# Optimization experiments

Hardware: AMD Instinct MI355X
Metric: run time of the kernel (lower is better)

Reference implementation:

```python
import jax, jax.numpy as jnp
import numpy as np

DIM = 256
H = 4
HD = DIM // H          # head_dim = 64
B = 4
N = 2048
M = 3                  # number of modalities
TEMP = 0.07
EPS = 1e-5             # torch LayerNorm eps


def _layernorm(x, g, b):
    mu = jnp.mean(x, axis=-1, keepdims=True)
    var = jnp.var(x, axis=-1, keepdims=True)  # biased, matches torch
    return (x - mu) / jnp.sqrt(var + EPS) * g + b


def setup_inputs() -> dict:
    key = jax.random.key(0)
    ks = jax.random.split(key, 8)
    s = 0.02
    return {
        "m0": jax.random.normal(ks[0], (B, N, DIM), jnp.float32),
        "m1": jax.random.normal(ks[1], (B, N, DIM), jnp.float32),
        "m2": jax.random.normal(ks[2], (B, N, DIM), jnp.float32),
        # torch Linear weights are [out, in]; applied as x @ W.T
        "Wq": jax.random.normal(ks[3], (DIM, DIM), jnp.float32) * s,
        "Wk": jax.random.normal(ks[4], (DIM, DIM), jnp.float32) * s,
        "Wv": jax.random.normal(ks[5], (DIM, DIM), jnp.float32) * s,
        "g1": jnp.ones((DIM,), jnp.float32),
        "be1": jnp.zeros((DIM,), jnp.float32),
        "W1": jax.random.normal(ks[6], (4 * DIM, DIM), jnp.float32) * s,
        "bm1": jnp.zeros((4 * DIM,), jnp.float32),
        "W2": jax.random.normal(ks[7], (DIM, 4 * DIM), jnp.float32) * s,
        "bm2": jnp.zeros((DIM,), jnp.float32),
        "g2": jnp.ones((DIM,), jnp.float32),
        "be2": jnp.zeros((DIM,), jnp.float32),
    }


def reference(m0, m1, m2, Wq, Wk, Wv, g1, be1, W1, bm1, W2, bm2, g2, be2):
    mods = jnp.stack([m0, m1, m2])  # [M, B, N, D]

    def proj(W):
        # x @ W.T, split heads -> [M, B, H, N, HD]
        y = jnp.einsum('mbnd,ed->mbne', mods, W)
        return y.reshape(M, B, N, H, HD).transpose(0, 1, 3, 2, 4)

    q, k, v = proj(Wq), proj(Wk), proj(Wv)
    scale = 1.0 / np.sqrt(HD).astype(np.float32)

    pair_loss = jnp.float32(0.0)
    updates = []
    for i in range(M):  # small fixed modality loop
        upd = jnp.zeros((B, N, DIM), mods.dtype)
        for j in range(M):
            # [B, H, N, N] cross-modal scores
            sim = jnp.einsum('bhnd,bhmd->bhnm', q[i], k[j]) * scale
            attn = jax.nn.softmax(sim, axis=-1)
            if i != j:
                diag = jnp.diagonal(sim, axis1=-2, axis2=-1)      # [B, H, N]
                lse = jax.nn.logsumexp(sim / TEMP, axis=-1)       # [B, H, N]
                pair_loss = pair_loss + jnp.mean(-diag + lse)
            au = jnp.einsum('bhnm,bhmd->bhnd', attn, v[j])
            upd = upd + au.transpose(0, 2, 1, 3).reshape(B, N, DIM)
        updates.append(upd)

    # original accumulates the pairwise loss once per outer modality, each
    # time divided by M*(M-1)  ->  total = M * pair_loss / (M*(M-1))
    total_loss = M * pair_loss / (M * (M - 1))

    outs = []
    for m in range(M):
        x = mods[m] + updates[m]
        x = _layernorm(x, g1, be1)
        h = jax.nn.gelu(x @ W1.T + bm1, approximate=False)  # exact GELU like torch
        x = x + (h @ W2.T + bm2)
        x = _layernorm(x, g2, be2)
        outs.append(x)

    return (outs[0], outs[1], outs[2], total_loss)
```

## Files before the change

### kernel.cpp

```cpp
#include <hip/hip_runtime.h>


typedef float f32x2 __attribute__((ext_vector_type(2)));
typedef float f32x4 __attribute__((ext_vector_type(4)));
typedef float f32x16 __attribute__((ext_vector_type(16)));
typedef __bf16 bf16x8 __attribute__((ext_vector_type(8)));
typedef unsigned int u32x2 __attribute__((ext_vector_type(2)));
typedef unsigned int u32x4 __attribute__((ext_vector_type(4)));
typedef unsigned short bfu4 __attribute__((ext_vector_type(4)));
typedef unsigned short bfu;

#define MFMA32(a, b, c) __builtin_amdgcn_mfma_f32_32x32x16_bf16(a, b, c, 0, 0, 0)

#define NTOK 2048
#define DIMM 256
#define HDIM 64
#define DFF 1024
#define OUT_LOSS 6291456
#define INVT 14.285714285714286f
#define LN2F 0.6931471805599453f
#define LOG2EF 1.4426950408889634f

#define EXP2F(x) __builtin_amdgcn_exp2f(x)
#define LOG2F(x) __builtin_amdgcn_logf(x)

__device__ __forceinline__ bfu f2bf(float f) {
  unsigned u = __float_as_uint(f);
  u += 0x7FFFu + ((u >> 16) & 1u);
  return (bfu)(u >> 16);
}
__device__ __forceinline__ float frombf(bfu v) {
  return __uint_as_float(((unsigned)v) << 16);
}

__device__ __forceinline__ bf16x8 ldfrag(const bfu* p) {
  return __builtin_bit_cast(bf16x8, *reinterpret_cast<const u32x4*>(p));
}

__device__ __forceinline__ unsigned pkbf(float lo, float hi) {
  unsigned d;
  asm("v_cvt_pk_bf16_f32 %0, %1, %2" : "=v"(d) : "v"(lo), "v"(hi));
  return d;
}
__device__ __forceinline__ void swap32u(unsigned& a, unsigned& b) {
  asm("v_permlane32_swap_b32 %0, %1" : "+v"(a), "+v"(b));
}
__device__ __forceinline__ float red32_add(float x) {
  float y = x;
  asm("v_permlane32_swap_b32 %0, %1" : "+v"(x), "+v"(y));
  return x + y;
}
__device__ __forceinline__ float red32_max(float x) {
  float y = x;
  asm("v_permlane32_swap_b32 %0, %1" : "+v"(x), "+v"(y));
  return fmaxf(x, y);
}

__global__ __launch_bounds__(256) void k_cvt_all(
    const float* __restrict__ m0, const float* __restrict__ m1,
    const float* __restrict__ m2, const float* __restrict__ Wq,
    const float* __restrict__ Wk, const float* __restrict__ Wv,
    const float* __restrict__ W1, const float* __restrict__ W2,
    bfu* __restrict__ Xb, bfu* __restrict__ Wqkv,
    bfu* __restrict__ W1b, bfu* __restrict__ W2b) {
  const int bid = blockIdx.x, tid = threadIdx.x;
  const float* src;
  bfu* dst;
  int idx;
  if (bid < 6144) {
    const int seg = bid >> 11;
    src = (seg == 0) ? m0 : (seg == 1 ? m1 : m2);
    dst = Xb + (size_t)seg * 2097152;
    idx = (bid & 2047) * 256 + tid;
  } else if (bid < 6336) {
    const int wseg = (bid - 6144) >> 6;
    src = (wseg == 0) ? Wq : (wseg == 1 ? Wk : Wv);
    dst = Wqkv + (size_t)wseg * 65536;
    idx = ((bid - 6144) & 63) * 256 + tid;
  } else if (bid < 6592) {
    src = W1; dst = W1b; idx = (bid - 6336) * 256 + tid;
  } else {
    src = W2; dst = W2b; idx = (bid - 6592) * 256 + tid;
  }
  f32x4 v = reinterpret_cast<const f32x4*>(src)[idx];
  bfu4 o;
  o[0] = f2bf(v[0]); o[1] = f2bf(v[1]); o[2] = f2bf(v[2]); o[3] = f2bf(v[3]);
  reinterpret_cast<bfu4*>(dst)[idx] = o;
}

#define RROW(r) (((r) & 3) + 8 * ((r) >> 2) + 4 * hi)

__global__ __launch_bounds__(256) void k_proj(const bfu* __restrict__ Xb,
                                              const bfu* __restrict__ Wcat,
                                              bfu* __restrict__ Qb,
                                              bfu* __restrict__ Kb,
                                              bfu* __restrict__ VTb) {
  __shared__ __align__(16) bfu sA[128][72];
  __shared__ __align__(16) bfu sB[128][72];
  const int tid = threadIdx.x;
  const int lane = tid & 63, w = tid >> 6;
  const int l31 = lane & 31, hi = lane >> 5, hi8 = hi * 8;
  const int wm = w >> 1, wn = w & 1;
  const int row0 = blockIdx.x * 128;
  const int col0 = blockIdx.y * 128;
  const bfu* Ap = Xb + (size_t)row0 * 256;
  const bfu* Bp = Wcat + (size_t)col0 * 256;
  f32x16 acc00 = {}, acc01 = {}, acc10 = {}, acc11 = {};
  u32x4 rA[4], rB[4];
#pragma unroll
  for (int t = 0; t < 4; ++t) {
    const int c = tid + 256 * t;
    rA[t] = *reinterpret_cast<const u32x4*>(Ap + (size_t)(c >> 3) * 256 + (c & 7) * 8);
    rB[t] = *reinterpret_cast<const u32x4*>(Bp + (size_t)(c >> 3) * 256 + (c & 7) * 8);
  }
#pragma unroll
  for (int ks = 0; ks < 4; ++ks) {
    __syncthreads();
#pragma unroll
    for (int t = 0; t < 4; ++t) {
      const int c = tid + 256 * t;
      *reinterpret_cast<u32x4*>(&sA[c >> 3][(c & 7) * 8]) = rA[t];
      *reinterpret_cast<u32x4*>(&sB[c >> 3][(c & 7) * 8]) = rB[t];
    }
    __syncthreads();
    if (ks < 3) {
      const int k0 = (ks + 1) * 64;
#pragma unroll
      for (int t = 0; t < 4; ++t) {
        const int c = tid + 256 * t;
        rA[t] = *reinterpret_cast<const u32x4*>(Ap + (size_t)(c >> 3) * 256 + k0 + (c & 7) * 8);
        rB[t] = *reinterpret_cast<const u32x4*>(Bp + (size_t)(c >> 3) * 256 + k0 + (c & 7) * 8);
      }
    }
#pragma unroll
    for (int kk = 0; kk < 4; ++kk) {
      bf16x8 a0 = ldfrag(&sA[wm * 64 + l31][kk * 16 + hi8]);
      bf16x8 a1 = ldfrag(&sA[wm * 64 + 32 + l31][kk * 16 + hi8]);
      bf16x8 b0 = ldfrag(&sB[wn * 64 + l31][kk * 16 + hi8]);
      bf16x8 b1 = ldfrag(&sB[wn * 64 + 32 + l31][kk * 16 + hi8]);
      acc00 = MFMA32(a0, b0, acc00);
      acc01 = MFMA32(a0, b1, acc01);
      acc10 = MFMA32(a1, b0, acc10);
      acc11 = MFMA32(a1, b1, acc11);
    }
  }
  const int mb = row0 >> 11;
  const int cb = col0 + wn * 64;
  const int which = cb >> 8;
  const int h = (cb >> 6) & 3;
  const size_t obase = ((size_t)mb * 4 + h) * ((size_t)NTOK * HDIM);
  const int tokb = (row0 & 2047) + wm * 64;
  const float qs = (which == 0) ? 0.125f * LOG2EF : 1.0f;
#define STORE_QK(ACC, MT, NT)                                                 \
  {                                                                           \
    bfu* dst = (which ? Kb : Qb) + obase;                                     \
    _Pragma("unroll") for (int r = 0; r < 16; ++r) {                          \
      const int tok = tokb + (MT) * 32 + RROW(r);                             \
      dst[(size_t)tok * 64 + (NT) * 32 + l31] = f2bf((ACC)[r] * qs);          \
    }                                                                         \
  }
#define STORE_VT(ACC, MT, NT)                                                 \
  {                                                                           \
    _Pragma("unroll") for (int g = 0; g < 4; ++g) {                           \
      bfu4 pk;                                                                \
      _Pragma("unroll") for (int q = 0; q < 4; ++q) pk[q] = f2bf((ACC)[4 * g + q]); \
      const int tok = tokb + (MT) * 32 + 8 * g + 4 * hi;                      \
      *reinterpret_cast<bfu4*>(                                               \
          &VTb[obase + (size_t)((NT) * 32 + l31) * NTOK + tok]) = pk;         \
    }                                                                         \
  }
  if (which < 2) {
    STORE_QK(acc00, 0, 0) STORE_QK(acc01, 0, 1)
    STORE_QK(acc10, 1, 0) STORE_QK(acc11, 1, 1)
  } else {
    STORE_VT(acc00, 0, 0) STORE_VT(acc01, 0, 1)
    STORE_VT(acc10, 1, 0) STORE_VT(acc11, 1, 1)
  }
}

__global__ __launch_bounds__(256) void k_ffn1(const bfu* __restrict__ x1b,
                                              const bfu* __restrict__ W1b,
                                              const float* __restrict__ bm1,
                                              bfu* __restrict__ hb) {
  __shared__ __align__(16) bfu sA[128][72];
  __shared__ __align__(16) bfu sB[128][72];
  const int tid = threadIdx.x;
  const int lane = tid & 63, w = tid >> 6;
  const int l31 = lane & 31, hi = lane >> 5, hi8 = hi * 8;
  const int wm = w >> 1, wn = w & 1;
  const int row0 = blockIdx.x * 128;
  const int col0 = blockIdx.y * 128;
  const bfu* Ap = x1b + (size_t)row0 * 256;
  const bfu* Bp = W1b + (size_t)col0 * 256;
  f32x16 acc00 = {}, acc01 = {}, acc10 = {}, acc11 = {};
  u32x4 rA[4], rB[4];
#pragma unroll
  for (int t = 0; t < 4; ++t) {
    const int c = tid + 256 * t;
    rA[t] = *reinterpret_cast<const u32x4*>(Ap + (size_t)(c >> 3) * 256 + (c & 7) * 8);
    rB[t] = *reinterpret_cast<const u32x4*>(Bp + (size_t)(c >> 3) * 256 + (c & 7) * 8);
  }
#pragma unroll
  for (int ks = 0; ks < 4; ++ks) {
    __syncthreads();
#pragma unroll
    for (int t = 0; t < 4; ++t) {
      const int c = tid + 256 * t;
      *reinterpret_cast<u32x4*>(&sA[c >> 3][(c & 7) * 8]) = rA[t];
      *reinterpret_cast<u32x4*>(&sB[c >> 3][(c & 7) * 8]) = rB[t];
    }
    __syncthreads();
    if (ks < 3) {
      const int k0 = (ks + 1) * 64;
#pragma unroll
      for (int t = 0; t < 4; ++t) {
        const int c = tid + 256 * t;
        rA[t] = *reinterpret_cast<const u32x4*>(Ap + (size_t)(c >> 3) * 256 + k0 + (c & 7) * 8);
        rB[t] = *reinterpret_cast<const u32x4*>(Bp + (size_t)(c >> 3) * 256 + k0 + (c & 7) * 8);
      }
    }
#pragma unroll
    for (int kk = 0; kk < 4; ++kk) {
      bf16x8 a0 = ldfrag(&sA[wm * 64 + l31][kk * 16 + hi8]);
      bf16x8 a1 = ldfrag(&sA[wm * 64 + 32 + l31][kk * 16 + hi8]);
      bf16x8 b0 = ldfrag(&sB[wn * 64 + l31][kk * 16 + hi8]);
      bf16x8 b1 = ldfrag(&sB[wn * 64 + 32 + l31][kk * 16 + hi8]);
      acc00 = MFMA32(a0, b0, acc00);
      acc01 = MFMA32(a0, b1, acc01);
      acc10 = MFMA32(a1, b0, acc10);
      acc11 = MFMA32(a1, b1, acc11);
    }
  }
  const int tokb = row0 + wm * 64;
#define STORE_H(ACC, MT, NT)                                                  \
  {                                                                           \
    const int e = col0 + wn * 64 + (NT) * 32 + l31;                           \
    const float bias = bm1[e];                                                \
    _Pragma("unroll") for (int r = 0; r < 16; ++r) {                          \
      const int tok = tokb + (MT) * 32 + RROW(r);                             \
      float v = (ACC)[r] + bias;                                              \
      v = 0.5f * v * (1.0f + erff(v * 0.70710678118f));                       \
      hb[(size_t)tok * DFF + e] = f2bf(v);                                    \
    }                                                                         \
  }
  STORE_H(acc00, 0, 0) STORE_H(acc01, 0, 1)
  STORE_H(acc10, 1, 0) STORE_H(acc11, 1, 1)
}

__global__ __launch_bounds__(256) void k_ffn2(const bfu* __restrict__ hb,
                                              const bfu* __restrict__ W2b,
                                              const float* __restrict__ bm2,
                                              const bfu* __restrict__ x1b,
                                              float* __restrict__ x2f) {
  __shared__ __align__(16) bfu sA[128][72];
  __shared__ __align__(16) bfu sB[64][72];
  const int tid = threadIdx.x;
  const int lane = tid & 63, w = tid >> 6;
  const int l31 = lane & 31, hi = lane >> 5, hi8 = hi * 8;
  const int row0 = blockIdx.x * 128;
  const int col0 = blockIdx.y * 64;
  const bfu* Ap = hb + (size_t)row0 * DFF;
  const bfu* Bp = W2b + (size_t)col0 * DFF;
  f32x16 acc0 = {}, acc1 = {};
  u32x4 rA[4], rB[2];
#pragma unroll
  for (int t = 0; t < 4; ++t) {
    const int c = tid + 256 * t;
    rA[t] = *reinterpret_cast<const u32x4*>(Ap + (size_t)(c >> 3) * DFF + (c & 7) * 8);
  }
#pragma unroll
  for (int t = 0; t < 2; ++t) {
    const int c = tid + 256 * t;
    rB[t] = *reinterpret_cast<const u32x4*>(Bp + (size_t)(c >> 3) * DFF + (c & 7) * 8);
  }
  for (int ks = 0; ks < 16; ++ks) {
    __syncthreads();
#pragma unroll
    for (int t = 0; t < 4; ++t) {
      const int c = tid + 256 * t;
      *reinterpret_cast<u32x4*>(&sA[c >> 3][(c & 7) * 8]) = rA[t];
    }
#pragma unroll
    for (int t = 0; t < 2; ++t) {
      const int c = tid + 256 * t;
      *reinterpret_cast<u32x4*>(&sB[c >> 3][(c & 7) * 8]) = rB[t];
    }
    __syncthreads();
    if (ks < 15) {
      const int k0 = (ks + 1) * 64;
#pragma unroll
      for (int t = 0; t < 4; ++t) {
        const int c = tid + 256 * t;
        rA[t] = *reinterpret_cast<const u32x4*>(Ap + (size_t)(c >> 3) * DFF + k0 + (c & 7) * 8);
      }
#pragma unroll
      for (int t = 0; t < 2; ++t) {
        const int c = tid + 256 * t;
        rB[t] = *reinterpret_cast<const u32x4*>(Bp + (size_t)(c >> 3) * DFF + k0 + (c & 7) * 8);
      }
    }
#pragma unroll
    for (int kk = 0; kk < 4; ++kk) {
      bf16x8 a = ldfrag(&sA[w * 32 + l31][kk * 16 + hi8]);
      bf16x8 b0 = ldfrag(&sB[l31][kk * 16 + hi8]);
      bf16x8 b1 = ldfrag(&sB[32 + l31][kk * 16 + hi8]);
      acc0 = MFMA32(a, b0, acc0);
      acc1 = MFMA32(a, b1, acc1);
    }
  }
  const int tokb = row0 + w * 32;
#define STORE_Y(ACC, NT)                                                      \
  {                                                                           \
    const int e = col0 + (NT) * 32 + l31;                                     \
    const float bias = bm2[e];                                                \
    _Pragma("unroll") for (int r = 0; r < 16; ++r) {                          \
      const int tok = tokb + RROW(r);                                         \
      x2f[(size_t)tok * DIMM + e] =                                           \
          (ACC)[r] + bias + frombf(x1b[(size_t)tok * DIMM + e]);              \
    }                                                                         \
  }
  STORE_Y(acc0, 0) STORE_Y(acc1, 1)
}

__global__ __launch_bounds__(256, 3) void k_attn(const bfu* __restrict__ Qb,
                                                 const bfu* __restrict__ Kb,
                                                 const bfu* __restrict__ VTb,
                                                 bfu* __restrict__ upd3,
                                                 float* __restrict__ lossbuf) {
  __shared__ __align__(16) bfu sK[2][64][72];
  __shared__ __align__(16) bfu sV[2][64][72];
  __shared__ float sRed[4];
  const int tid = threadIdx.x;
  const int lane = tid & 63, w = tid >> 6;
  const int l31 = lane & 31, hi = lane >> 5;
  const int hi8 = hi * 8;
  const int qt = blockIdx.x, bh = blockIdx.y, ij = blockIdx.z;
  const int i = ij / 3, j = ij % 3;
  const bool wl = (i != j);
  const int b = bh >> 2, h = bh & 3;
  const int q0 = qt * 128 + w * 32;
  const int q = q0 + l31;
  const int ktd = q0 >> 6;
  const size_t plane = (size_t)NTOK * HDIM;
  const size_t qoff = (((size_t)i * 4 + b) * 4 + h) * plane;
  const size_t kvoff = (((size_t)j * 4 + b) * 4 + h) * plane;
  const bfu* Kp = Kb + kvoff;
  const bfu* Vp = VTb + kvoff;
  const int r0 = tid >> 2, c0 = (tid & 3) * 2;

  bf16x8 qf[4];
#pragma unroll
  for (int c = 0; c < 4; ++c)
    qf[c] = ldfrag(Qb + qoff + (size_t)q * HDIM + c * 16 + hi8);

  float lossacc = 0.0f;
  float mrun = -1e30f, lrun = 0.0f, l2run = 0.0f;
  f32x16 O0 = {}, O1 = {};
  u32x4 pk0, pk1, pv0, pv1;

#define ISSUE_TILE(K0)                                                       \
    {                                                                        \
      const bfu* kp_ = Kp + (size_t)((K0) + r0) * HDIM + c0 * 8;             \
      pk0 = *reinterpret_cast<const u32x4*>(kp_);                            \
      pk1 = *reinterpret_cast<const u32x4*>(kp_ + 8);                        \
      const bfu* vp_ = Vp + (size_t)r0 * NTOK + (K0) + c0 * 8;               \
      pv0 = *reinterpret_cast<const u32x4*>(vp_);                            \
      pv1 = *reinterpret_cast<const u32x4*>(vp_ + 8);                        \
    }
#define WRITE_TILE(BUF)                                                      \
    {                                                                        \
      *reinterpret_cast<u32x4*>(&sK[BUF][r0][c0 * 8]) = pk0;                 \
      *reinterpret_cast<u32x4*>(&sK[BUF][r0][c0 * 8 + 8]) = pk1;             \
      *reinterpret_cast<u32x4*>(&sV[BUF][r0][c0 * 8]) = pv0;                 \
      *reinterpret_cast<u32x4*>(&sV[BUF][r0][c0 * 8 + 8]) = pv1;             \
    }

  ISSUE_TILE(0);
  WRITE_TILE(0);
  __syncthreads();
  int cur = 0;

  for (int kt = 0; kt < 32; ++kt) {
    if (kt < 31) ISSUE_TILE((kt + 1) * 64);

    f32x16 S0 = {}, S1 = {};
    __builtin_amdgcn_s_setprio(1);
#pragma unroll
    for (int c = 0; c < 4; ++c) {
      bf16x8 a0 = ldfrag(&sK[cur][l31][c * 16 + hi8]);
      bf16x8 a1 = ldfrag(&sK[cur][32 + l31][c * 16 + hi8]);
      S0 = MFMA32(a0, qf[c], S0);
      S1 = MFMA32(a1, qf[c], S1);
    }
    __builtin_amdgcn_s_setprio(0);

    if (wl) {
      if (kt == ktd) {
#pragma unroll
        for (int r = 0; r < 16; ++r) {
          const int klow = (r & 3) + 8 * (r >> 2) + 4 * hi;
          const float sv = (w & 1) ? S1[r] : S0[r];
          if (klow == l31) lossacc -= sv * LN2F;
        }
      }
      float pmax = -1e30f;
#pragma unroll
      for (int r = 0; r < 16; ++r) pmax = fmaxf(pmax, fmaxf(S0[r], S1[r]));
      pmax = red32_max(pmax);
      if (__any(pmax > mrun + 1.9f)) {
        const float mnew = fmaxf(mrun, pmax);
        l2run *= EXP2F((mrun - mnew) * INVT);
        mrun = mnew;
      }
    }

    const float mI = mrun * INVT;
    f32x2 psv = {};
    f32x2 p2v = {};
#pragma unroll
    for (int r = 0; r < 16; ++r) {
      const float e0 = EXP2F(S0[r]), e1 = EXP2F(S1[r]);
      f32x2 ev; ev[0] = e0; ev[1] = e1;
      psv += ev;
      if (wl) {
        f32x2 pv2;
        pv2[0] = EXP2F(fmaf(S0[r], INVT, -mI));
        pv2[1] = EXP2F(fmaf(S1[r], INVT, -mI));
        p2v += pv2;
      }
      S0[r] = e0; S1[r] = e1;
    }
    lrun += red32_add(psv[0] + psv[1]);
    if (wl) l2run += red32_add(p2v[0] + p2v[1]);

    __builtin_amdgcn_s_setprio(1);
#pragma unroll
    for (int c = 0; c < 4; ++c) {
      const int half = c >> 1, sub = c & 1;
      unsigned q01, q23, q45, q67;
      if (half == 0) {
        q01 = pkbf(S0[sub * 8 + 0], S0[sub * 8 + 1]);
        q23 = pkbf(S0[sub * 8 + 2], S0[sub * 8 + 3]);
        q45 = pkbf(S0[sub * 8 + 4], S0[sub * 8 + 5]);
        q67 = pkbf(S0[sub * 8 + 6], S0[sub * 8 + 7]);
      } else {
        q01 = pkbf(S1[sub * 8 + 0], S1[sub * 8 + 1]);
        q23 = pkbf(S1[sub * 8 + 2], S1[sub * 8 + 3]);
        q45 = pkbf(S1[sub * 8 + 4], S1[sub * 8 + 5]);
        q67 = pkbf(S1[sub * 8 + 6], S1[sub * 8 + 7]);
      }
      swap32u(q01, q45);
      swap32u(q23, q67);
      u32x4 bb; bb[0] = q01; bb[1] = q23; bb[2] = q45; bb[3] = q67;
      const bf16x8 pb = __builtin_bit_cast(bf16x8, bb);
      bf16x8 a0 = ldfrag(&sV[cur][l31][c * 16 + hi8]);
      bf16x8 a1 = ldfrag(&sV[cur][32 + l31][c * 16 + hi8]);
      O0 = MFMA32(a0, pb, O0);
      O1 = MFMA32(a1, pb, O1);
    }
    __builtin_amdgcn_s_setprio(0);

    if (kt < 31) WRITE_TILE(cur ^ 1);
    __syncthreads();
    cur ^= 1;
  }

  const float inv = 1.0f / lrun;
  bfu* up = upd3 + ((size_t)((j * 3 + i) * 4 + b) * NTOK + q) * DIMM + h * 64;
#pragma unroll
  for (int g = 0; g < 4; ++g) {
    u32x2 st0, st1;
    st0[0] = pkbf(O0[4 * g + 0] * inv, O0[4 * g + 1] * inv);
    st0[1] = pkbf(O0[4 * g + 2] * inv, O0[4 * g + 3] * inv);
    st1[0] = pkbf(O1[4 * g + 0] * inv, O1[4 * g + 1] * inv);
    st1[1] = pkbf(O1[4 * g + 2] * inv, O1[4 * g + 3] * inv);
    *reinterpret_cast<u32x2*>(up + 8 * g + 4 * hi) = st0;
    *reinterpret_cast<u32x2*>(up + 32 + 8 * g + 4 * hi) = st1;
  }
  if (wl && hi == 0)
    lossacc += LN2F * (mrun * INVT + LOG2F(l2run));

  float v = lossacc;
#pragma unroll
  for (int mk = 1; mk < 64; mk <<= 1) v += __shfl_xor(v, mk);
  if (lane == 0) sRed[w] = v;
  __syncthreads();
  if (tid == 0)
    lossbuf[((size_t)ij * 16 + bh) * 16 + qt] =
        sRed[0] + sRed[1] + sRed[2] + sRed[3];
}

__global__ __launch_bounds__(256) void k_ln1(const float* __restrict__ m0,
                                             const float* __restrict__ m1,
                                             const float* __restrict__ m2,
                                             const bfu* __restrict__ upd3,
                                             const float* __restrict__ g1,
                                             const float* __restrict__ be1,
                                             bfu* __restrict__ x1b) {
  const int tid = threadIdx.x;
  const int lane = tid & 63, w = tid >> 6;
  const int row = blockIdx.x * 4 + w;
  const int i = row >> 13;
  const int rr = row & 8191;
  const float* src = (i == 0 ? m0 : (i == 1 ? m1 : m2)) + (size_t)rr * DIMM;
  f32x4 x = *reinterpret_cast<const f32x4*>(src + lane * 4);
#pragma unroll
  for (int j = 0; j < 3; ++j) {
    bfu4 uv = *reinterpret_cast<const bfu4*>(
        upd3 + ((size_t)(j * 3 + i) * 8192 + rr) * DIMM + lane * 4);
#pragma unroll
    for (int qi = 0; qi < 4; ++qi) x[qi] += frombf(uv[qi]);
  }
  float s = x[0] + x[1] + x[2] + x[3];
  float s2 = x[0] * x[0] + x[1] * x[1] + x[2] * x[2] + x[3] * x[3];
#pragma unroll
  for (int mk = 1; mk < 64; mk <<= 1) { s += __shfl_xor(s, mk); s2 += __shfl_xor(s2, mk); }
  const float mu = s * (1.0f / 256.0f);
  const float var = s2 * (1.0f / 256.0f) - mu * mu;
  const float rstd = rsqrtf(var + 1e-5f);
  f32x4 g = *reinterpret_cast<const f32x4*>(g1 + lane * 4);
  f32x4 bb = *reinterpret_cast<const f32x4*>(be1 + lane * 4);
  bfu4 ob;
#pragma unroll
  for (int qi = 0; qi < 4; ++qi)
    ob[qi] = f2bf((x[qi] - mu) * rstd * g[qi] + bb[qi]);
  *reinterpret_cast<bfu4*>(x1b + (size_t)row * DIMM + lane * 4) = ob;
}

__global__ __launch_bounds__(256) void k_ln2(const float* __restrict__ x2f,
                                             const float* __restrict__ g2,
                                             const float* __restrict__ be2,
                                             float* __restrict__ out) {
  const int tid = threadIdx.x;
  const int lane = tid & 63, w = tid >> 6;
  const int row = blockIdx.x * 4 + w;
  f32x4 x = *reinterpret_cast<const f32x4*>(x2f + (size_t)row * DIMM + lane * 4);
  float s = x[0] + x[1] + x[2] + x[3];
  float s2 = x[0] * x[0] + x[1] * x[1] + x[2] * x[2] + x[3] * x[3];
#pragma unroll
  for (int mk = 1; mk < 64; mk <<= 1) { s += __shfl_xor(s, mk); s2 += __shfl_xor(s2, mk); }
  const float mu = s * (1.0f / 256.0f);
  const float var = s2 * (1.0f / 256.0f) - mu * mu;
  const float rstd = rsqrtf(var + 1e-5f);
  f32x4 g = *reinterpret_cast<const f32x4*>(g2 + lane * 4);
  f32x4 bb = *reinterpret_cast<const f32x4*>(be2 + lane * 4);
  f32x4 o;
#pragma unroll
  for (int qi = 0; qi < 4; ++qi) o[qi] = (x[qi] - mu) * rstd * g[qi] + bb[qi];
  *reinterpret_cast<f32x4*>(out + (size_t)row * DIMM + lane * 4) = o;
}

__global__ __launch_bounds__(256) void k_loss(const float* __restrict__ lossbuf,
                                              float* __restrict__ out) {
  __shared__ float red[4];
  const int tid = threadIdx.x;
  float s = 0.0f;
  for (int idx = tid; idx < 2304; idx += 256) s += lossbuf[idx];
#pragma unroll
  for (int mk = 1; mk < 64; mk <<= 1) s += __shfl_xor(s, mk);
  if ((tid & 63) == 0) red[tid >> 6] = s;
  __syncthreads();
  if (tid == 0)
    out[OUT_LOSS] = (red[0] + red[1] + red[2] + red[3]) * (1.0f / (32768.0f * 2.0f));
}

extern "C" void kernel_launch(void* const* d_in, const int* in_sizes, int n_in,
                              void* d_out, int out_size, void* d_ws, size_t ws_size,
                              hipStream_t stream) {
  const float* m0 = (const float*)d_in[0];
  const float* m1 = (const float*)d_in[1];
  const float* m2 = (const float*)d_in[2];
  const float* Wq = (const float*)d_in[3];
  const float* Wk = (const float*)d_in[4];
  const float* Wv = (const float*)d_in[5];
  const float* g1 = (const float*)d_in[6];
  const float* be1 = (const float*)d_in[7];
  const float* W1 = (const float*)d_in[8];
  const float* bm1 = (const float*)d_in[9];
  const float* W2 = (const float*)d_in[10];
  const float* bm2 = (const float*)d_in[11];
  const float* g2 = (const float*)d_in[12];
  const float* be2 = (const float*)d_in[13];
  float* out = (float*)d_out;

  char* ws = (char*)d_ws;
  bfu* Xb   = (bfu*)(ws + 0);
  bfu* Wqkv = (bfu*)(ws + 12582912);
  bfu* Qb   = (bfu*)(ws + 12976128);
  bfu* Kb   = (bfu*)(ws + 25559040);
  bfu* VTb  = (bfu*)(ws + 38141952);
  bfu* Hb   = (bfu*)(ws + 0);
  bfu* upd3 = (bfu*)(ws + 50724864);
  float* x2f = (float*)(ws + 50724864);
  bfu* x1b  = (bfu*)(ws + 88473600);
  bfu* W1b  = (bfu*)(ws + 101056512);
  bfu* W2b  = (bfu*)(ws + 101580800);
  float* lossbuf = (float*)(ws + 102105088);

  k_cvt_all<<<6848, 256, 0, stream>>>(m0, m1, m2, Wq, Wk, Wv, W1, W2,
                                      Xb, Wqkv, W1b, W2b);

  k_proj<<<dim3(192, 6), 256, 0, stream>>>(Xb, Wqkv, Qb, Kb, VTb);
  k_attn<<<dim3(16, 16, 9), 256, 0, stream>>>(Qb, Kb, VTb, upd3, lossbuf);
  k_ln1<<<6144, 256, 0, stream>>>(m0, m1, m2, upd3, g1, be1, x1b);
  k_ffn1<<<dim3(192, 8), 256, 0, stream>>>(x1b, W1b, bm1, Hb);
  k_ffn2<<<dim3(192, 4), 256, 0, stream>>>(Hb, W2b, bm2, x1b, x2f);
  k_ln2<<<6144, 256, 0, stream>>>(x2f, g2, be2, out);
  k_loss<<<1, 256, 0, stream>>>(lossbuf, out);
}
```

Measured before the change: 313.9 us.

## Stage attention K/V tiles via direct global-to-LDS loads with XOR swizzle

Measured after the change: 350.7 us. +11.7%, slower.

```diff
diff --git a/kernel.cpp b/kernel.cpp
--- a/kernel.cpp
+++ b/kernel.cpp
@@ -35,6 +35,12 @@
 
 __device__ __forceinline__ bf16x8 ldfrag(const bfu* p) {
   return __builtin_bit_cast(bf16x8, *reinterpret_cast<const u32x4*>(p));
+}
+
+__device__ __forceinline__ void gl16(const bfu* g, bfu* l) {
+  __builtin_amdgcn_global_load_lds(
+      (const __attribute__((address_space(1))) unsigned int*)g,
+      (__attribute__((address_space(3))) unsigned int*)l, 16, 0, 0);
 }
 
 __device__ __forceinline__ unsigned pkbf(float lo, float hi) {
@@ -322,13 +328,13 @@
   STORE_Y(acc0, 0) STORE_Y(acc1, 1)
 }
 
-__global__ __launch_bounds__(256, 3) void k_attn(const bfu* __restrict__ Qb,
+__global__ __launch_bounds__(256, 4) void k_attn(const bfu* __restrict__ Qb,
                                                  const bfu* __restrict__ Kb,
                                                  const bfu* __restrict__ VTb,
                                                  bfu* __restrict__ upd3,
                                                  float* __restrict__ lossbuf) {
-  __shared__ __align__(16) bfu sK[2][64][72];
-  __shared__ __align__(16) bfu sV[2][64][72];
+  __shared__ __align__(16) bfu sK[2][64][64];
+  __shared__ __align__(16) bfu sV[2][64][64];
   __shared__ float sRed[4];
   const int tid = threadIdx.x;
   const int lane = tid & 63, w = tid >> 6;
@@ -346,7 +352,13 @@
   const size_t kvoff = (((size_t)j * 4 + b) * 4 + h) * plane;
   const bfu* Kp = Kb + kvoff;
   const bfu* Vp = VTb + kvoff;
-  const int r0 = tid >> 2, c0 = (tid & 3) * 2;
+
+  const int r0_ = w * 16 + (lane >> 3);
+  const int c0_ = ((lane & 7) ^ (r0_ & 7)) * 8;
+  const bfu* KpS0 = Kp + (size_t)r0_ * HDIM + c0_;
+  const bfu* KpS1 = Kp + (size_t)(r0_ + 8) * HDIM + c0_;
+  const bfu* VpS0 = Vp + (size_t)r0_ * NTOK + c0_;
+  const bfu* VpS1 = Vp + (size_t)(r0_ + 8) * NTOK + c0_;
 
   bf16x8 qf[4];
 #pragma unroll
@@ -356,39 +368,29 @@
   float lossacc = 0.0f;
   float mrun = -1e30f, lrun = 0.0f, l2run = 0.0f;
   f32x16 O0 = {}, O1 = {};
-  u32x4 pk0, pk1, pv0, pv1;
-
-#define ISSUE_TILE(K0)                                                       \
+  const int sw = (l31 & 7) * 8;
+
+#define STAGE(K0, BUF)                                                       \
     {                                                                        \
-      const bfu* kp_ = Kp + (size_t)((K0) + r0) * HDIM + c0 * 8;             \
-      pk0 = *reinterpret_cast<const u32x4*>(kp_);                            \
-      pk1 = *reinterpret_cast<const u32x4*>(kp_ + 8);                        \
-      const bfu* vp_ = Vp + (size_t)r0 * NTOK + (K0) + c0 * 8;               \
-      pv0 = *reinterpret_cast<const u32x4*>(vp_);                            \
-      pv1 = *reinterpret_cast<const u32x4*>(vp_ + 8);                        \
-    }
-#define WRITE_TILE(BUF)                                                      \
-    {                                                                        \
-      *reinterpret_cast<u32x4*>(&sK[BUF][r0][c0 * 8]) = pk0;                 \
-      *reinterpret_cast<u32x4*>(&sK[BUF][r0][c0 * 8 + 8]) = pk1;             \
-      *reinterpret_cast<u32x4*>(&sV[BUF][r0][c0 * 8]) = pv0;                 \
-      *reinterpret_cast<u32x4*>(&sV[BUF][r0][c0 * 8 + 8]) = pv1;             \
-    }
-
-  ISSUE_TILE(0);
-  WRITE_TILE(0);
+      gl16(KpS0 + (size_t)(K0) * HDIM, &sK[BUF][w * 16][0]);                 \
+      gl16(KpS1 + (size_t)(K0) * HDIM, &sK[BUF][w * 16 + 8][0]);             \
+      gl16(VpS0 + (K0), &sV[BUF][w * 16][0]);                                \
+      gl16(VpS1 + (K0), &sV[BUF][w * 16 + 8][0]);                            \
+    }
+
+  STAGE(0, 0);
   __syncthreads();
   int cur = 0;
 
   for (int kt = 0; kt < 32; ++kt) {
-    if (kt < 31) ISSUE_TILE((kt + 1) * 64);
+    if (kt < 31) STAGE((kt + 1) * 64, cur ^ 1);
 
     f32x16 S0 = {}, S1 = {};
     __builtin_amdgcn_s_setprio(1);
 #pragma unroll
     for (int c = 0; c < 4; ++c) {
-      bf16x8 a0 = ldfrag(&sK[cur][l31][c * 16 + hi8]);
-      bf16x8 a1 = ldfrag(&sK[cur][32 + l31][c * 16 + hi8]);
+      bf16x8 a0 = ldfrag(&sK[cur][l31][(c * 16 + hi8) ^ sw]);
+      bf16x8 a1 = ldfrag(&sK[cur][32 + l31][(c * 16 + hi8) ^ sw]);
       S0 = MFMA32(a0, qf[c], S0);
       S1 = MFMA32(a1, qf[c], S1);
     }
@@ -453,14 +455,13 @@
       swap32u(q23, q67);
       u32x4 bb; bb[0] = q01; bb[1] = q23; bb[2] = q45; bb[3] = q67;
       const bf16x8 pb = __builtin_bit_cast(bf16x8, bb);
-      bf16x8 a0 = ldfrag(&sV[cur][l31][c * 16 + hi8]);
-      bf16x8 a1 = ldfrag(&sV[cur][32 + l31][c * 16 + hi8]);
+      bf16x8 a0 = ldfrag(&sV[cur][l31][(c * 16 + hi8) ^ sw]);
+      bf16x8 a1 = ldfrag(&sV[cur][32 + l31][(c * 16 + hi8) ^ sw]);
       O0 = MFMA32(a0, pb, O0);
       O1 = MFMA32(a1, pb, O1);
     }
     __builtin_amdgcn_s_setprio(0);
 
-    if (kt < 31) WRITE_TILE(cur ^ 1);
     __syncthreads();
     cur ^= 1;
   }
```
